# Performance work log

Hardware: AMD Instinct MI355X
Metric: run time of the kernel (lower is better)

Reference implementation:

```python
import jax, jax.numpy as jnp
import numpy as np

B, L, D_E = 2, 2048, 1024
H, D_Q = 16, 64
EPS = 1e-5


def setup_inputs() -> dict:
    key = jax.random.key(0)
    ks = jax.random.split(key, 12)
    s_in = 1.0 / np.sqrt(D_E)
    s_mid = 1.0 / np.sqrt(H * D_Q)
    return {
        "pre_q": jax.random.normal(ks[0], (B, L, D_E), jnp.float32),
        "pre_k": jax.random.normal(ks[1], (B, L, D_E), jnp.float32),
        "Wq": jax.random.normal(ks[2], (D_E, H * D_Q), jnp.float32) * s_in,
        "bq": jnp.zeros((H * D_Q,), jnp.float32),
        "Wk": jax.random.normal(ks[3], (D_E, H * D_Q), jnp.float32) * s_in,
        "bk": jnp.zeros((H * D_Q,), jnp.float32),
        "Wv": jax.random.normal(ks[4], (D_E, H * D_Q), jnp.float32) * s_in,
        "bv": jnp.zeros((H * D_Q,), jnp.float32),
        "Wo": jax.random.normal(ks[5], (H * D_Q, D_E), jnp.float32) * s_mid,
        "bo": jnp.zeros((D_E,), jnp.float32),
        "gamma": jnp.ones((D_E,), jnp.float32),
        "beta": jnp.zeros((D_E,), jnp.float32),
    }


def reference(pre_q, pre_k, Wq, bq, Wk, bk, Wv, bv, Wo, bo, gamma, beta):
    b, ql, _ = pre_q.shape
    kl = pre_k.shape[1]
    q = (pre_q @ Wq + bq).reshape(b, ql, H, D_Q)
    k = (pre_k @ Wk + bk).reshape(b, kl, H, D_Q)
    v = (pre_k @ Wv + bv).reshape(b, kl, H, D_Q)
    scores = jnp.einsum('bqhd,bkhd->bhqk', q, k) / jnp.sqrt(jnp.float32(D_Q))
    attn = jax.nn.softmax(scores, axis=-1)
    ctx = jnp.einsum('bhqk,bkhd->bqhd', attn, v).reshape(b, ql, H * D_Q)
    out = ctx @ Wo + bo
    x = pre_q + out
    mu = jnp.mean(x, axis=-1, keepdims=True)
    var = jnp.mean(jnp.square(x - mu), axis=-1, keepdims=True)
    return (x - mu) * jax.lax.rsqrt(var + EPS) * gamma + beta
```

## Files before the change

### kernel.cpp

```cpp
#include <hip/hip_runtime.h>
#include <hip/hip_bf16.h>
#include <cstdint>

typedef unsigned short ushort_t;
typedef __attribute__((ext_vector_type(8))) short short8;
typedef __attribute__((ext_vector_type(8))) __bf16 bf16x8;
typedef __attribute__((ext_vector_type(4))) float f32x4;
typedef __attribute__((ext_vector_type(4))) ushort_t ushort4v;
typedef __attribute__((ext_vector_type(2))) unsigned int uint2v;
typedef __attribute__((ext_vector_type(4))) unsigned int uint4v;

__device__ inline ushort_t f2bf(float f) {
    union { float f; unsigned u; } x; x.f = f;
    unsigned r = x.u + 0x7fffu + ((x.u >> 16) & 1u);
    return (ushort_t)(r >> 16);
}

__device__ inline unsigned pkbf(float a, float b) {
    __hip_bfloat162 h = __float22bfloat162_rn(float2{a, b});
    unsigned r;
    __builtin_memcpy(&r, &h, 4);
    return r;
}

__device__ inline float bf2f(ushort_t u) {
    unsigned v = (unsigned)u << 16;
    return __builtin_bit_cast(float, v);
}

__device__ inline unsigned pktrunc(float a, float b) {
    return __builtin_amdgcn_perm(__builtin_bit_cast(unsigned, b),
                                 __builtin_bit_cast(unsigned, a), 0x07060302u);
}

#if __has_builtin(__builtin_amdgcn_exp2f)
#define EXP2(x) __builtin_amdgcn_exp2f(x)
#else
#define EXP2(x) __builtin_exp2f(x)
#endif

__device__ inline bf16x8 ldfrag(const ushort_t* p) {
    short8 s = *(const short8*)p;
    return __builtin_bit_cast(bf16x8, s);
}

__device__ inline f32x4 mfma16(bf16x8 a, bf16x8 b, f32x4 c) {
    return __builtin_amdgcn_mfma_f32_16x16x32_bf16(a, b, c, 0, 0, 0);
}

__device__ inline void glds16(const ushort_t* g, ushort_t* l) {
    __builtin_amdgcn_global_load_lds((const __attribute__((address_space(1))) void*)g,
                                     (__attribute__((address_space(3))) void*)l, 16, 0, 0);
}

__global__ __launch_bounds__(256) void prep_k(const float* __restrict__ W0, const float* __restrict__ W1,
                                              const float* __restrict__ W2, const float* __restrict__ W3,
                                              ushort_t* __restrict__ wout) {
    const int blk = blockIdx.x;
    const int t = threadIdx.x;
    const int z = blk >> 10;
    const int bx = (blk & 31) * 32, by = ((blk >> 5) & 31) * 32;
    const float* W = (z == 0) ? W0 : (z == 1) ? W1 : (z == 2) ? W2 : W3;
    ushort_t* o = wout + (size_t)z * (1u << 20);
    __shared__ float tile[32][33];
    const int tx = t & 31, ty = t >> 5;
#pragma unroll
    for (int r = 0; r < 4; ++r)
        tile[ty + r * 8][tx] = W[(size_t)(by + ty + r * 8) * 1024 + bx + tx];
    __syncthreads();
#pragma unroll
    for (int r = 0; r < 4; ++r)
        o[(size_t)(bx + ty + r * 8) * 1024 + by + tx] = f2bf(tile[tx][ty + r * 8]);
}

template <int MODE>
__global__ __launch_bounds__(256) void gemm128(
    const float* __restrict__ Af1, const float* __restrict__ Af2,
    const ushort_t* __restrict__ A1,
    const ushort_t* __restrict__ Wt,
    const float* __restrict__ bias0, const float* __restrict__ bias1, const float* __restrict__ bias2,
    ushort_t* __restrict__ oQ, ushort_t* __restrict__ oK, ushort_t* __restrict__ oVt,
    const float* __restrict__ resid, ushort_t* __restrict__ oXb) {
    const int t = threadIdx.x;
    const int phys = blockIdx.x;
    const int bid = (MODE == 0) ? (phys & 7) * 96 + (phys >> 3)
                                : (phys & 7) * 32 + (phys >> 3);
    int g, mb, nb;
    const float* bias;
    const ushort_t* Wg;
    if (MODE == 0) {
        g = bid >> 8;
        const int rem = bid & 255;
        mb = rem >> 3;
        nb = rem & 7;
        Wg = Wt + (size_t)g * (1u << 20);
        bias = (g == 0) ? bias0 : (g == 1) ? bias1 : bias2;
    } else {
        g = 0;
        mb = bid >> 3;
        nb = bid & 7;
        Wg = Wt;
        bias = bias0;
    }
    const int m0 = mb * 128, n0 = nb * 128;

    __shared__ ushort_t As[3][128 * 32];
    __shared__ ushort_t Bs[3][128 * 32];
    const int row4 = t >> 2, c8 = (t & 3) * 8;
    const ushort_t* Bg = Wg + (size_t)(n0 + row4) * 1024 + c8;
    const int ldst = row4 * 32 + c8;

    const float* Agf = nullptr;
    const ushort_t* Ag = nullptr;
    if (MODE == 0)
        Agf = ((g == 0) ? Af1 : Af2) + (size_t)(m0 + row4) * 1024 + c8;
    else
        Ag = A1 + (size_t)(m0 + row4) * 1024 + c8;

    const int lane = t & 63, wid = t >> 6;
    const int wm = wid >> 1, wn = wid & 1;
    const int lr = lane & 15, lgp = lane >> 4, lk = lgp * 8;

    f32x4 acc[4][4];
#pragma unroll
    for (int j = 0; j < 4; ++j) {
        const f32x4 bj = *(const f32x4*)(bias + n0 + wn * 64 + j * 16 + 4 * lgp);
#pragma unroll
        for (int i = 0; i < 4; ++i) acc[j][i] = bj;
    }

    f32x4 a0, a1, a2, a3;

#define A_LOAD(kt)                                              \
    {                                                           \
        a0 = *(const f32x4*)(Agf + (kt));                       \
        a1 = *(const f32x4*)(Agf + (kt) + 4);                   \
        a2 = *(const f32x4*)(Agf + (kt) + 64 * 1024);           \
        a3 = *(const f32x4*)(Agf + (kt) + 64 * 1024 + 4);       \
    }

#define A_WRITE(buf)                                                               \
    {                                                                              \
        uint4v w0 = {pkbf(a0[0], a0[1]), pkbf(a0[2], a0[3]),                       \
                     pkbf(a1[0], a1[1]), pkbf(a1[2], a1[3])};                      \
        *(uint4v*)&As[buf][ldst] = w0;                                             \
        uint4v w1 = {pkbf(a2[0], a2[1]), pkbf(a2[2], a2[3]),                       \
                     pkbf(a3[0], a3[1]), pkbf(a3[2], a3[3])};                      \
        *(uint4v*)&As[buf][ldst + 2048] = w1;                                      \
    }

#define B_STAGE(buf, kt)                                        \
    {                                                           \
        glds16(Bg + (kt), &Bs[buf][ldst]);                      \
        glds16(Bg + (kt) + 64 * 1024, &Bs[buf][ldst + 2048]);   \
    }

#define A_STAGE_G(buf, kt)                                      \
    {                                                           \
        glds16(Ag + (kt), &As[buf][ldst]);                      \
        glds16(Ag + (kt) + 64 * 1024, &As[buf][ldst + 2048]);   \
    }

#define COMPUTE(buf)                                                              \
    {                                                                             \
        bf16x8 af[4], bfr[4];                                                     \
        _Pragma("unroll") for (int i = 0; i < 4; ++i)                             \
            af[i] = ldfrag(&As[buf][(wm * 64 + i * 16 + lr) * 32 + lk]);          \
        _Pragma("unroll") for (int j = 0; j < 4; ++j)                             \
            bfr[j] = ldfrag(&Bs[buf][(wn * 64 + j * 16 + lr) * 32 + lk]);         \
        __builtin_amdgcn_s_setprio(1);                                            \
        _Pragma("unroll") for (int j = 0; j < 4; ++j)                             \
            _Pragma("unroll") for (int i = 0; i < 4; ++i)                         \
                acc[j][i] = mfma16(bfr[j], af[i], acc[j][i]);                     \
        __builtin_amdgcn_s_setprio(0);                                            \
    }

#define GITER0(it, buf, buf2)                                                     \
    {                                                                             \
        if ((it) <= 30) { asm volatile("s_waitcnt vmcnt(2)" ::: "memory"); }      \
        else            { asm volatile("s_waitcnt vmcnt(0)" ::: "memory"); }      \
        A_WRITE(buf)                                                              \
        __syncthreads();                                                          \
        if ((it) + 1 < 32) A_LOAD(((it) + 1) * 32)                                \
        if ((it) + 2 < 32) B_STAGE(buf2, ((it) + 2) * 32)                         \
        COMPUTE(buf)                                                              \
    }

#define GITER1(it, buf, buf2)                                                     \
    {                                                                             \
        if ((it) <= 30) { asm volatile("s_waitcnt vmcnt(4)" ::: "memory"); }      \
        else            { asm volatile("s_waitcnt vmcnt(0)" ::: "memory"); }      \
        __syncthreads();                                                          \
        if ((it) + 2 < 32) { A_STAGE_G(buf2, ((it) + 2) * 32) B_STAGE(buf2, ((it) + 2) * 32) } \
        COMPUTE(buf)                                                              \
    }

    if (MODE == 0) {
        B_STAGE(0, 0);
        A_LOAD(0);
        B_STAGE(1, 32);
        for (int b3 = 0; b3 < 30; b3 += 3) {
            GITER0(b3 + 0, 0, 2)
            GITER0(b3 + 1, 1, 0)
            GITER0(b3 + 2, 2, 1)
        }
        GITER0(30, 0, 2)
        GITER0(31, 1, 0)
    } else {
        A_STAGE_G(0, 0) B_STAGE(0, 0);
        A_STAGE_G(1, 32) B_STAGE(1, 32);
        for (int b3 = 0; b3 < 30; b3 += 3) {
            GITER1(b3 + 0, 0, 2)
            GITER1(b3 + 1, 1, 0)
            GITER1(b3 + 2, 2, 1)
        }
        GITER1(30, 0, 2)
        GITER1(31, 1, 0)
    }
#undef A_LOAD
#undef A_WRITE
#undef B_STAGE
#undef A_STAGE_G
#undef COMPUTE
#undef GITER0
#undef GITER1

    const float qs = (MODE == 0 && g == 0) ? 0.18033688011f : 1.0f;

#pragma unroll
    for (int j = 0; j < 4; ++j) {
        const int n = n0 + wn * 64 + j * 16 + 4 * lgp;
#pragma unroll
        for (int i = 0; i < 4; ++i) {
            const f32x4 v = acc[j][i];
            const int m = m0 + wm * 64 + i * 16 + lr;
            if (MODE == 0) {
                const int b = m >> 11, ll = m & 2047;
                const int h = n >> 6, d = n & 63;
                if (g == 2) {
                    const int lp = (ll & ~63) | (ll & 32) | (((ll >> 2) & 3) << 3)
                                 | (((ll >> 4) & 1) << 2) | (ll & 3);
#pragma unroll
                    for (int jj = 0; jj < 4; ++jj)
                        oVt[((size_t)(b * 16 + h) * 64 + d + jj) * 2048 + lp] = f2bf(v[jj]);
                } else {
                    uint2v cw = {pkbf(v[0] * qs, v[1] * qs), pkbf(v[2] * qs, v[3] * qs)};
                    ushort_t* dst = (g == 0) ? oQ : oK;
                    *(uint2v*)(dst + (((size_t)(b * 16 + h) * 2048) + ll) * 64 + d) = cw;
                }
            } else {
                const float4 r = *(const float4*)(resid + (size_t)m * 1024 + n);
                uint2v cw = {pkbf(v[0] + r.x, v[1] + r.y), pkbf(v[2] + r.z, v[3] + r.w)};
                *(uint2v*)(oXb + (size_t)m * 1024 + n) = cw;
            }
        }
    }
}

__global__ __launch_bounds__(256, 2) void attn_k(const ushort_t* __restrict__ Qg, const ushort_t* __restrict__ Kg,
                                                 const ushort_t* __restrict__ Vtg, ushort_t* __restrict__ Cg) {
    __shared__ ushort_t Ks[4][8 * 512];
    __shared__ ushort_t Vs[4][8 * 512];

    const int t = threadIdx.x;
    const int lane = t & 63, w = t >> 6;
    const int bid = blockIdx.x;
    const int xcd = bid & 7, j = bid >> 3;
    const int bh = (xcd << 2) | (j >> 4);
    const int qb = j & 15;
    const int q0 = qb * 128 + w * 32;
    const int lr = lane & 15, g = lane >> 4;
    const int srow = lane & 15, sch = lane >> 4;

    const ushort_t* Kbase = Kg + (size_t)bh * (2048 * 64);
    const ushort_t* Vbase = Vtg + (size_t)bh * (64 * 2048);

    const ushort_t* QpA = Qg + ((size_t)bh * 2048 + q0 + lr) * 64 + g * 8;
    const bf16x8 qA0 = ldfrag(QpA), qA1 = ldfrag(QpA + 32);
    const bf16x8 qB0 = ldfrag(QpA + 16 * 64), qB1 = ldfrag(QpA + 16 * 64 + 32);

    f32x4 oA[4] = {}, oB[4] = {};
    float lA = 0.f, lB = 0.f;

#define STAGE(buf, kt)                                                                        \
    {                                                                                         \
        glds16(Kbase + (size_t)((kt) + 16 * w + srow) * 64 + sch * 8, &Ks[buf][w * 512 + lane * 8]);            \
        glds16(Kbase + (size_t)((kt) + 16 * w + srow) * 64 + 32 + sch * 8, &Ks[buf][(4 + w) * 512 + lane * 8]); \
        glds16(Vbase + (size_t)(16 * w + srow) * 2048 + (kt) + sch * 8, &Vs[buf][(2 * w) * 512 + lane * 8]);    \
        glds16(Vbase + (size_t)(16 * w + srow) * 2048 + (kt) + 32 + sch * 8, &Vs[buf][(2 * w + 1) * 512 + lane * 8]); \
    }

#define COMPUTE(BUF)                                                                      \
    {                                                                                     \
        f32x4 stA[4], stB[4];                                                             \
        _Pragma("unroll") for (int f = 0; f < 4; ++f) {                                   \
            const bf16x8 k0 = ldfrag(&Ks[BUF][f * 512 + lane * 8]);                       \
            const bf16x8 k1 = ldfrag(&Ks[BUF][(4 + f) * 512 + lane * 8]);                 \
            f32x4 sA = {}, sB = {};                                                       \
            sA = mfma16(k0, qA0, sA);                                                     \
            sA = mfma16(k1, qA1, sA);                                                     \
            sB = mfma16(k0, qB0, sB);                                                     \
            sB = mfma16(k1, qB1, sB);                                                     \
            stA[f] = sA;                                                                  \
            stB[f] = sB;                                                                  \
        }                                                                                 \
        unsigned pkA[8], pkB[8];                                                          \
        float rsA = 0.f, rsB = 0.f;                                                       \
        _Pragma("unroll") for (int f = 0; f < 4; ++f) {                                   \
            const float a0 = EXP2(stA[f][0]);                                             \
            const float a1 = EXP2(stA[f][1]);                                             \
            const float a2 = EXP2(stA[f][2]);                                             \
            const float a3 = EXP2(stA[f][3]);                                             \
            rsA += (a0 + a1) + (a2 + a3);                                                 \
            pkA[2 * f] = pktrunc(a0, a1);                                                 \
            pkA[2 * f + 1] = pktrunc(a2, a3);                                             \
            const float b0 = EXP2(stB[f][0]);                                             \
            const float b1 = EXP2(stB[f][1]);                                             \
            const float b2 = EXP2(stB[f][2]);                                             \
            const float b3 = EXP2(stB[f][3]);                                             \
            rsB += (b0 + b1) + (b2 + b3);                                                 \
            pkB[2 * f] = pktrunc(b0, b1);                                                 \
            pkB[2 * f + 1] = pktrunc(b2, b3);                                             \
        }                                                                                 \
        lA += rsA;                                                                        \
        lB += rsB;                                                                        \
        _Pragma("unroll") for (int b = 0; b < 2; ++b) {                                   \
            const uint4v ua = {pkA[4 * b], pkA[4 * b + 1], pkA[4 * b + 2], pkA[4 * b + 3]}; \
            const uint4v ub = {pkB[4 * b], pkB[4 * b + 1], pkB[4 * b + 2], pkB[4 * b + 3]}; \
            const bf16x8 pA = __builtin_bit_cast(bf16x8, ua);                             \
            const bf16x8 pB = __builtin_bit_cast(bf16x8, ub);                             \
            _Pragma("unroll") for (int df = 0; df < 4; ++df) {                            \
                const bf16x8 vf = ldfrag(&Vs[BUF][(2 * df + b) * 512 + (g * 16 + lr) * 8]); \
                oA[df] = mfma16(vf, pA, oA[df]);                                          \
                oB[df] = mfma16(vf, pB, oB[df]);                                          \
            }                                                                             \
        }                                                                                 \
    }

    STAGE(0, 0);
    STAGE(1, 64);
    asm volatile("s_waitcnt vmcnt(0)" ::: "memory");
    __syncthreads();

    for (int kt4 = 0; kt4 < 2048; kt4 += 256) {
        if (kt4 + 128 < 2048) {
            STAGE(2, kt4 + 128);
            STAGE(3, kt4 + 192);
        }
        if (w < 2) { COMPUTE(0) COMPUTE(1) }
        else       { COMPUTE(1) COMPUTE(0) }
        asm volatile("s_waitcnt vmcnt(0)" ::: "memory");
        __syncthreads();
        if (kt4 + 256 < 2048) {
            STAGE(0, kt4 + 256);
            STAGE(1, kt4 + 320);
        }
        if (w < 2) { COMPUTE(2) COMPUTE(3) }
        else       { COMPUTE(3) COMPUTE(2) }
        asm volatile("s_waitcnt vmcnt(0)" ::: "memory");
        __syncthreads();
    }
#undef STAGE
#undef COMPUTE

    lA += __shfl_xor(lA, 16, 64);
    lA += __shfl_xor(lA, 32, 64);
    lB += __shfl_xor(lB, 16, 64);
    lB += __shfl_xor(lB, 32, 64);

    const int bb = bh >> 4, hh = bh & 15;
    {
        const float inv = 1.0f / lA;
        ushort_t* cp = Cg + ((size_t)(bb * 2048 + q0 + lr) * 1024) + hh * 64;
#pragma unroll
        for (int df = 0; df < 4; ++df) {
            uint2v cw = {pkbf(oA[df][0] * inv, oA[df][1] * inv), pkbf(oA[df][2] * inv, oA[df][3] * inv)};
            *(uint2v*)(cp + 16 * df + 4 * g) = cw;
        }
    }
    {
        const float inv = 1.0f / lB;
        ushort_t* cp = Cg + ((size_t)(bb * 2048 + q0 + 16 + lr) * 1024) + hh * 64;
#pragma unroll
        for (int df = 0; df < 4; ++df) {
            uint2v cw = {pkbf(oB[df][0] * inv, oB[df][1] * inv), pkbf(oB[df][2] * inv, oB[df][3] * inv)};
            *(uint2v*)(cp + 16 * df + 4 * g) = cw;
        }
    }
}

__global__ __launch_bounds__(256) void ln_k(const ushort_t* __restrict__ X, const float* __restrict__ gamma,
                                            const float* __restrict__ beta, float* __restrict__ out) {
    const int row = blockIdx.x, t = threadIdx.x;
    const ushort4v xr = ((const ushort4v*)(X + (size_t)row * 1024))[t];
    const float x0 = bf2f(xr[0]), x1 = bf2f(xr[1]), x2 = bf2f(xr[2]), x3 = bf2f(xr[3]);
    float s = (x0 + x1) + (x2 + x3);
    float s2 = (x0 * x0 + x1 * x1) + (x2 * x2 + x3 * x3);
#pragma unroll
    for (int m = 1; m < 64; m <<= 1) {
        s += __shfl_xor(s, m, 64);
        s2 += __shfl_xor(s2, m, 64);
    }
    __shared__ float rs[4], rq[4];
    if ((t & 63) == 0) { rs[t >> 6] = s; rq[t >> 6] = s2; }
    __syncthreads();
    const float S = rs[0] + rs[1] + rs[2] + rs[3];
    const float S2 = rq[0] + rq[1] + rq[2] + rq[3];
    const float mu = S * (1.0f / 1024.0f);
    const float var = S2 * (1.0f / 1024.0f) - mu * mu;
    const float r = rsqrtf(var + 1e-5f);
    const float4 gg = ((const float4*)gamma)[t];
    const float4 bb = ((const float4*)beta)[t];
    float4 o;
    o.x = (x0 - mu) * r * gg.x + bb.x;
    o.y = (x1 - mu) * r * gg.y + bb.y;
    o.z = (x2 - mu) * r * gg.z + bb.z;
    o.w = (x3 - mu) * r * gg.w + bb.w;
    ((float4*)(out + (size_t)row * 1024))[t] = o;
}

extern "C" void kernel_launch(void* const* d_in, const int* in_sizes, int n_in,
                              void* d_out, int out_size, void* d_ws, size_t ws_size,
                              hipStream_t stream) {
    (void)in_sizes; (void)n_in; (void)out_size; (void)ws_size;
    const float* pre_q = (const float*)d_in[0];
    const float* pre_k = (const float*)d_in[1];
    const float* Wq = (const float*)d_in[2];
    const float* bq = (const float*)d_in[3];
    const float* Wk = (const float*)d_in[4];
    const float* bk = (const float*)d_in[5];
    const float* Wv = (const float*)d_in[6];
    const float* bv = (const float*)d_in[7];
    const float* Wo = (const float*)d_in[8];
    const float* bo = (const float*)d_in[9];
    const float* gamma = (const float*)d_in[10];
    const float* beta = (const float*)d_in[11];
    float* out = (float*)d_out;
    char* ws = (char*)d_ws;
    const size_t MB = 1024 * 1024;
    ushort_t* Wt = (ushort_t*)(ws + 16 * MB);
    ushort_t* Qb = (ushort_t*)(ws + 24 * MB);
    ushort_t* Kb = (ushort_t*)(ws + 32 * MB);
    ushort_t* Vt = (ushort_t*)(ws + 40 * MB);
    ushort_t* CTX = (ushort_t*)(ws + 48 * MB);
    ushort_t* Xres = (ushort_t*)(ws);

    prep_k<<<4096, 256, 0, stream>>>(Wq, Wk, Wv, Wo, Wt);
    gemm128<0><<<768, 256, 0, stream>>>(pre_q, pre_k, nullptr, Wt, bq, bk, bv,
                                        Qb, Kb, Vt, nullptr, nullptr);
    attn_k<<<512, 256, 0, stream>>>(Qb, Kb, Vt, CTX);
    gemm128<1><<<256, 256, 0, stream>>>(nullptr, nullptr, CTX, Wt + 3 * (1u << 20), bo, nullptr, nullptr,
                                        nullptr, nullptr, nullptr, pre_q, Xres);
    ln_k<<<4096, 256, 0, stream>>>(Xres, gamma, beta, out);
}
```

Measured before the change: 121.5 us.

## Restructure fp32-input projection GEMM pipeline into 64-wide K steps with staggered wave order

The fp32-A projection path now processes two 32-wide K slices per iteration. It holds both slices' A data in registers, double-buffers the B tiles in a single shared LDS array, and synchronises twice per step. Waves 0-1 and 2-3 consume the two sub-slices in opposite order, which spreads LDS fragment reads and MFMA issue across the barrier interval. The intent is to amortise the wait/convert/barrier overhead over larger K chunks. The cost is a full vmcnt(0) wait each step, so memory-latency hiding may be shallower, and more registers are used for the second A stage.

```diff
diff --git a/kernel.cpp b/kernel.cpp
--- a/kernel.cpp
+++ b/kernel.cpp
@@ -104,8 +104,7 @@
     }
     const int m0 = mb * 128, n0 = nb * 128;
 
-    __shared__ ushort_t As[3][128 * 32];
-    __shared__ ushort_t Bs[3][128 * 32];
+    __shared__ ushort_t SH[6 * 4096];
     const int row4 = t >> 2, c8 = (t & 3) * 8;
     const ushort_t* Bg = Wg + (size_t)(n0 + row4) * 1024 + c8;
     const int ldst = row4 * 32 + c8;
@@ -129,45 +128,54 @@
         for (int i = 0; i < 4; ++i) acc[j][i] = bj;
     }
 
-    f32x4 a0, a1, a2, a3;
-
-#define A_LOAD(kt)                                              \
+    f32x4 aE0, aE1, aE2, aE3;
+    f32x4 aO0, aO1, aO2, aO3;
+
+#define ASB(i) (SH + (i) * 4096)
+#define BSB(i) (SH + (2 + (i)) * 4096)
+#define BSB1(i) (SH + (3 + (i)) * 4096)
+
+#define A_LOAD_E(kt)                                            \
     {                                                           \
-        a0 = *(const f32x4*)(Agf + (kt));                       \
-        a1 = *(const f32x4*)(Agf + (kt) + 4);                   \
-        a2 = *(const f32x4*)(Agf + (kt) + 64 * 1024);           \
-        a3 = *(const f32x4*)(Agf + (kt) + 64 * 1024 + 4);       \
-    }
-
-#define A_WRITE(buf)                                                               \
+        aE0 = *(const f32x4*)(Agf + (kt));                      \
+        aE1 = *(const f32x4*)(Agf + (kt) + 4);                  \
+        aE2 = *(const f32x4*)(Agf + (kt) + 64 * 1024);          \
+        aE3 = *(const f32x4*)(Agf + (kt) + 64 * 1024 + 4);      \
+    }
+#define A_LOAD_O(kt)                                            \
+    {                                                           \
+        aO0 = *(const f32x4*)(Agf + (kt));                      \
+        aO1 = *(const f32x4*)(Agf + (kt) + 4);                  \
+        aO2 = *(const f32x4*)(Agf + (kt) + 64 * 1024);          \
+        aO3 = *(const f32x4*)(Agf + (kt) + 64 * 1024 + 4);      \
+    }
+#define A_WRITE_TO(base, r0, r1, r2, r3)                                           \
     {                                                                              \
-        uint4v w0 = {pkbf(a0[0], a0[1]), pkbf(a0[2], a0[3]),                       \
-                     pkbf(a1[0], a1[1]), pkbf(a1[2], a1[3])};                      \
-        *(uint4v*)&As[buf][ldst] = w0;                                             \
-        uint4v w1 = {pkbf(a2[0], a2[1]), pkbf(a2[2], a2[3]),                       \
-                     pkbf(a3[0], a3[1]), pkbf(a3[2], a3[3])};                      \
-        *(uint4v*)&As[buf][ldst + 2048] = w1;                                      \
-    }
-
-#define B_STAGE(buf, kt)                                        \
+        uint4v w0 = {pkbf(r0[0], r0[1]), pkbf(r0[2], r0[3]),                       \
+                     pkbf(r1[0], r1[1]), pkbf(r1[2], r1[3])};                      \
+        *(uint4v*)((base) + ldst) = w0;                                            \
+        uint4v w1 = {pkbf(r2[0], r2[1]), pkbf(r2[2], r2[3]),                       \
+                     pkbf(r3[0], r3[1]), pkbf(r3[2], r3[3])};                      \
+        *(uint4v*)((base) + ldst + 2048) = w1;                                     \
+    }
+#define B_STAGE_TO(base, kt)                                    \
     {                                                           \
-        glds16(Bg + (kt), &Bs[buf][ldst]);                      \
-        glds16(Bg + (kt) + 64 * 1024, &Bs[buf][ldst + 2048]);   \
-    }
-
-#define A_STAGE_G(buf, kt)                                      \
+        glds16(Bg + (kt), (base) + ldst);                       \
+        glds16(Bg + (kt) + 64 * 1024, (base) + ldst + 2048);    \
+    }
+#define A_STAGE_G(base, kt)                                     \
     {                                                           \
-        glds16(Ag + (kt), &As[buf][ldst]);                      \
-        glds16(Ag + (kt) + 64 * 1024, &As[buf][ldst + 2048]);   \
-    }
-
-#define COMPUTE(buf)                                                              \
+        glds16(Ag + (kt), (base) + ldst);                       \
+        glds16(Ag + (kt) + 64 * 1024, (base) + ldst + 2048);    \
+    }
+
+#define COMPUTE_AT(abase, bbase)                                                  \
     {                                                                             \
         bf16x8 af[4], bfr[4];                                                     \
         _Pragma("unroll") for (int i = 0; i < 4; ++i)                             \
-            af[i] = ldfrag(&As[buf][(wm * 64 + i * 16 + lr) * 32 + lk]);          \
+            af[i] = ldfrag((abase) + (wm * 64 + i * 16 + lr) * 32 + lk);          \
         _Pragma("unroll") for (int j = 0; j < 4; ++j)                             \
-            bfr[j] = ldfrag(&Bs[buf][(wn * 64 + j * 16 + lr) * 32 + lk]);         \
+            bfr[j] = ldfrag((bbase) + (wn * 64 + j * 16 + lr) * 32 + lk);         \
         __builtin_amdgcn_s_setprio(1);                                            \
         _Pragma("unroll") for (int j = 0; j < 4; ++j)                             \
             _Pragma("unroll") for (int i = 0; i < 4; ++i)                         \
@@ -175,40 +183,46 @@
         __builtin_amdgcn_s_setprio(0);                                            \
     }
 
-#define GITER0(it, buf, buf2)                                                     \
-    {                                                                             \
-        if ((it) <= 30) { asm volatile("s_waitcnt vmcnt(2)" ::: "memory"); }      \
-        else            { asm volatile("s_waitcnt vmcnt(0)" ::: "memory"); }      \
-        A_WRITE(buf)                                                              \
-        __syncthreads();                                                          \
-        if ((it) + 1 < 32) A_LOAD(((it) + 1) * 32)                                \
-        if ((it) + 2 < 32) B_STAGE(buf2, ((it) + 2) * 32)                         \
-        COMPUTE(buf)                                                              \
-    }
-
 #define GITER1(it, buf, buf2)                                                     \
     {                                                                             \
         if ((it) <= 30) { asm volatile("s_waitcnt vmcnt(4)" ::: "memory"); }      \
         else            { asm volatile("s_waitcnt vmcnt(0)" ::: "memory"); }      \
         __syncthreads();                                                          \
-        if ((it) + 2 < 32) { A_STAGE_G(buf2, ((it) + 2) * 32) B_STAGE(buf2, ((it) + 2) * 32) } \
-        COMPUTE(buf)                                                              \
+        if ((it) + 2 < 32) { A_STAGE_G(ASB(buf2), ((it) + 2) * 32) B_STAGE_TO(BSB1(buf2), ((it) + 2) * 32) } \
+        COMPUTE_AT(ASB(buf), BSB1(buf))                                           \
     }
 
     if (MODE == 0) {
-        B_STAGE(0, 0);
-        A_LOAD(0);
-        B_STAGE(1, 32);
-        for (int b3 = 0; b3 < 30; b3 += 3) {
-            GITER0(b3 + 0, 0, 2)
-            GITER0(b3 + 1, 1, 0)
-            GITER0(b3 + 2, 2, 1)
-        }
-        GITER0(30, 0, 2)
-        GITER0(31, 1, 0)
+        A_LOAD_E(0);
+        A_LOAD_O(32);
+        B_STAGE_TO(BSB(0), 0);
+        B_STAGE_TO(BSB(1), 32);
+        for (int s = 0; s < 16; ++s) {
+            const int kt = s * 64;
+            const int pb = (s & 1) * 2;
+            const int pn = 2 - pb;
+            asm volatile("s_waitcnt vmcnt(0)" ::: "memory");
+            A_WRITE_TO(ASB(0), aE0, aE1, aE2, aE3)
+            A_WRITE_TO(ASB(1), aO0, aO1, aO2, aO3)
+            __syncthreads();
+            if (s < 15) {
+                A_LOAD_E(kt + 64);
+                A_LOAD_O(kt + 96);
+                B_STAGE_TO(BSB(pn), kt + 64);
+                B_STAGE_TO(BSB(pn + 1), kt + 96);
+            }
+            if (wid < 2) {
+                COMPUTE_AT(ASB(0), BSB(pb))
+                COMPUTE_AT(ASB(1), BSB(pb + 1))
+            } else {
+                COMPUTE_AT(ASB(1), BSB(pb + 1))
+                COMPUTE_AT(ASB(0), BSB(pb))
+            }
+            __syncthreads();
+        }
     } else {
-        A_STAGE_G(0, 0) B_STAGE(0, 0);
-        A_STAGE_G(1, 32) B_STAGE(1, 32);
+        A_STAGE_G(ASB(0), 0) B_STAGE_TO(BSB1(0), 0);
+        A_STAGE_G(ASB(1), 32) B_STAGE_TO(BSB1(1), 32);
         for (int b3 = 0; b3 < 30; b3 += 3) {
             GITER1(b3 + 0, 0, 2)
             GITER1(b3 + 1, 1, 0)
@@ -217,12 +231,15 @@
         GITER1(30, 0, 2)
         GITER1(31, 1, 0)
     }
-#undef A_LOAD
-#undef A_WRITE
-#undef B_STAGE
+#undef ASB
+#undef BSB
+#undef BSB1
+#undef A_LOAD_E
+#undef A_LOAD_O
+#undef A_WRITE_TO
+#undef B_STAGE_TO
 #undef A_STAGE_G
-#undef COMPUTE
-#undef GITER0
+#undef COMPUTE_AT
 #undef GITER1
 
     const float qs = (MODE == 0 && g == 0) ? 0.18033688011f : 1.0f;
```

Measured after the change: 121.0 us. Within noise of the previous version (-0.5%).
